# Optimization experiments

Hardware: AMD Instinct MI355X
Metric: run time of the kernel (lower is better)

Reference implementation:

```python
import jax, jax.numpy as jnp
import numpy as np
import math

T, B, V, D = 8, 32, 50257, 256
N = 4096            # memory slots
H = 4               # attention heads
L = 2               # transformer layers
K = 3               # shift width
HALF = K // 2
WIN = 16            # controller window
RH, WH = 1, 1       # read / write heads
EPS = 1e-12


def _pe(win, d):
    pos = jnp.arange(win, dtype=jnp.float32)[:, None]
    div = jnp.exp(jnp.arange(0, d, 2, dtype=jnp.float32) * (-math.log(10000.0) / d))
    pe = jnp.zeros((win, d), dtype=jnp.float32)
    pe = pe.at[:, 0::2].set(jnp.sin(pos * div))
    pe = pe.at[:, 1::2].set(jnp.cos(pos * div))
    return pe[:, None, :]


def _ln(x, g, b, eps=1e-5):
    mu = x.mean(-1, keepdims=True)
    var = ((x - mu) ** 2).mean(-1, keepdims=True)
    return (x - mu) * jax.lax.rsqrt(var + eps) * g + b


def _mha(x, Wqkv, bqkv, Wo, bo):
    S, Bc, Dm = x.shape
    dh = Dm // H
    qkv = x @ Wqkv.T + bqkv
    q, k, v = jnp.split(qkv, 3, axis=-1)
    q = q.reshape(S, Bc, H, dh)
    k = k.reshape(S, Bc, H, dh)
    v = v.reshape(S, Bc, H, dh)
    logits = jnp.einsum('sbhd,tbhd->bhst', q, k) / math.sqrt(dh)
    a = jax.nn.softmax(logits, axis=-1)
    o = jnp.einsum('bhst,tbhd->sbhd', a, v).reshape(S, Bc, Dm)
    return o @ Wo.T + bo


def _addressing(key_v, beta, gate, shift, gamma, prev_w, memory):
    # key_v [B,M], beta/gate/gamma [B,1], shift [B,K], prev_w [B,N], memory [B,N,M]
    key_n = key_v / (jnp.linalg.norm(key_v, axis=-1, keepdims=True) + EPS)
    mem_n = memory / (jnp.linalg.norm(memory, axis=-1, keepdims=True) + EPS)
    cos = jnp.einsum('bnm,bm->bn', mem_n, key_n)
    wc = jax.nn.softmax(jax.nn.softplus(beta) * cos, axis=-1)
    g = jax.nn.sigmoid(gate)
    wg = g * wc + (1.0 - g) * prev_w
    s = jax.nn.softmax(shift, axis=-1)
    shifted = sum(s[:, k:k + 1] * jnp.roll(wg, k - HALF, axis=-1) for k in range(K))
    gp = 1.0 + jax.nn.softplus(gamma)
    wt = (shifted + EPS) ** gp
    return wt / (wt.sum(-1, keepdims=True) + EPS)


def setup_inputs() -> dict:
    key = jax.random.key(0)
    ks = iter(jax.random.split(key, 40))
    def w(shape, s=0.02):
        return jax.random.normal(next(ks), shape, jnp.float32) * s
    return {
        'tokens': jax.random.randint(next(ks), (T, B), 0, V, jnp.int32),
        'emb_W': w((V, D)),
        'read_gate_W': w((D, D)), 'read_gate_b': jnp.zeros((D,)),
        'film_W': w((2 * D, D)), 'film_b': jnp.zeros((2 * D,)),
        't_Wqkv': w((L, 3 * D, D)), 't_bqkv': jnp.zeros((L, 3 * D)),
        't_Wo': w((L, D, D)), 't_bo': jnp.zeros((L, D)),
        't_ln1_g': jnp.ones((L, D)), 't_ln1_b': jnp.zeros((L, D)),
        't_ln2_g': jnp.ones((L, D)), 't_ln2_b': jnp.zeros((L, D)),
        't_W1': w((L, 4 * D, D)), 't_b1': jnp.zeros((L, 4 * D)),
        't_W2': w((L, D, 4 * D)), 't_b2': jnp.zeros((L, D)),
        'out_ln_g': jnp.ones((D,)), 'out_ln_b': jnp.zeros((D,)),
        'lstm_Wih': w((2, 4 * D, D)), 'lstm_Whh': w((2, 4 * D, D)),
        'lstm_bih': jnp.zeros((2, 4 * D)), 'lstm_bhh': jnp.zeros((2, 4 * D)),
        'head_W': w((V, D)), 'head_b': jnp.zeros((V,)),
        'read_W': w((D + 3 + K, D)), 'read_b': jnp.zeros((D + 3 + K,)),
        'write_W': w((3 * D + 3 + K, D)), 'write_b': jnp.zeros((3 * D + 3 + K,)),
    }


def reference(tokens, emb_W, read_gate_W, read_gate_b, film_W, film_b,
              t_Wqkv, t_bqkv, t_Wo, t_bo, t_ln1_g, t_ln1_b, t_ln2_g, t_ln2_b,
              t_W1, t_b1, t_W2, t_b2, out_ln_g, out_ln_b,
              lstm_Wih, lstm_Whh, lstm_bih, lstm_bhh,
              head_W, head_b, read_W, read_b, write_W, write_b):
    pe = _pe(WIN, D)
    memory = jnp.zeros((B, N, D), jnp.float32)
    read_w = jnp.zeros((B, RH, N), jnp.float32).at[:, :, 0].set(1.0)
    write_w = jnp.zeros((B, WH, N), jnp.float32).at[:, :, 0].set(1.0)
    record = jnp.zeros((B, D), jnp.float32)
    hx = jnp.zeros((2, B, D), jnp.float32)
    cx = jnp.zeros((2, B, D), jnp.float32)
    hist = jnp.zeros((1, B, D), jnp.float32)
    logits_all = []
    for t in range(T):  # T fixed, sequential recurrence (context length grows)
        emb = emb_W[tokens[t]]                               # [B,D]
        r = jnp.einsum('bhn,bnm->bm', read_w, memory)        # sum over read heads
        fp = record @ film_W.T + film_b
        gam = 1.0 + jnp.tanh(fp[:, :D])
        bet = fp[:, D:]
        rg = jax.nn.sigmoid(record @ read_gate_W.T + read_gate_b)
        x_in = gam * emb + bet + rg * r
        ctx = jnp.concatenate([hist, x_in[None]], axis=0)
        if ctx.shape[0] > WIN:
            ctx = ctx[-WIN:]
        hist = ctx
        h = ctx + pe[:ctx.shape[0]]
        for l in range(L):  # norm_first pre-LN encoder layers (eval, relu FFN)
            h = h + _mha(_ln(h, t_ln1_g[l], t_ln1_b[l]), t_Wqkv[l], t_bqkv[l], t_Wo[l], t_bo[l])
            h = h + (jax.nn.relu(_ln(h, t_ln2_g[l], t_ln2_b[l]) @ t_W1[l].T + t_b1[l]) @ t_W2[l].T + t_b2[l])
        c_out = _ln(h[-1], out_ln_g, out_ln_b)
        # 2-layer LSTM single step (torch gate order i,f,g,o)
        x_l = c_out
        new_h, new_c = [], []
        for l in range(2):
            gates = x_l @ lstm_Wih[l].T + lstm_bih[l] + hx[l] @ lstm_Whh[l].T + lstm_bhh[l]
            i_g, f_g, g_g, o_g = jnp.split(gates, 4, axis=-1)
            c_new = jax.nn.sigmoid(f_g) * cx[l] + jax.nn.sigmoid(i_g) * jnp.tanh(g_g)
            h_new = jax.nn.sigmoid(o_g) * jnp.tanh(c_new)
            new_h.append(h_new); new_c.append(c_new)
            x_l = h_new
        hx = jnp.stack(new_h); cx = jnp.stack(new_c)
        record = hx[-1]
        c_out = c_out + x_l
        logits_all.append(c_out @ head_W.T + head_b)
        # read addressing
        rp = (c_out @ read_W.T + read_b).reshape(B, RH, -1)
        new_rw = []
        for hh in range(RH):
            p = rp[:, hh]
            new_rw.append(_addressing(p[:, :D], p[:, D:D + 1], p[:, D + 1:D + 2],
                                      p[:, D + 2:D + 2 + K], p[:, D + 2 + K:D + 3 + K],
                                      read_w[:, hh], memory))
        read_w = jnp.stack(new_rw, axis=1)
        # write addressing + erase/add (addressing uses pre-update memory)
        wp = (c_out @ write_W.T + write_b).reshape(B, WH, -1)
        mem_pre = memory
        new_ww = []
        for hh in range(WH):
            p = wp[:, hh]
            wt = _addressing(p[:, :D], p[:, D:D + 1], p[:, D + 1:D + 2],
                             p[:, D + 2:D + 2 + K], p[:, D + 2 + K:D + 3 + K],
                             write_w[:, hh], mem_pre)
            erase = jax.nn.sigmoid(p[:, D + 3 + K:2 * D + 3 + K])
            add = jnp.tanh(p[:, 2 * D + 3 + K:3 * D + 3 + K])
            memory = memory * (1.0 - wt[:, :, None] * erase[:, None, :]) + wt[:, :, None] * add[:, None, :]
            new_ww.append(wt)
        write_w = jnp.stack(new_ww, axis=1)
    return jnp.stack(logits_all, axis=0)  # [T, B, V]
```

## Files before the change

### kernel.cpp

```cpp
#include <hip/hip_runtime.h>
#include <math.h>

#define TT 8
#define BB 32
#define VV 50257
#define DD 256
#define NN 4096
#define EPS_ 1e-12f

typedef __attribute__((ext_vector_type(8))) short short8;
typedef __attribute__((ext_vector_type(4))) float f32x4;

__device__ __forceinline__ float sigf(float x) { return 1.f / (1.f + expf(-x)); }
__device__ __forceinline__ float softplusf_(float x) { return fmaxf(x, 0.f) + log1pf(expf(-fabsf(x))); }
__device__ __forceinline__ unsigned f2bf(float f) {
  union { float f; unsigned u; } c; c.f = f;
  return (c.u + 0x7FFFu + ((c.u >> 16) & 1u)) >> 16;
}
__device__ __forceinline__ float bf2f(unsigned u16) {
  union { unsigned u; float f; } c; c.u = u16 << 16; return c.f;
}

__device__ __forceinline__ float blk_sum(float v, float* s) {
#pragma unroll
// ... 42 lines not shown
  if (k == 0) cb[l * 1024 + np] = bih[l * 1024 + src] + bhh[l * 1024 + src];
}

__global__ void catrw_k(const float* __restrict__ rW, const float* __restrict__ rb,
                        const float* __restrict__ wW, const float* __restrict__ wb,
                        unsigned short* __restrict__ Wrw, float* __restrict__ brw) {
  int i = blockIdx.x * 256 + threadIdx.x;
  if (i >= 1036 * 256) return;
  int k = i & 255, n = i >> 8;
  float v = (n < 262) ? rW[(size_t)n * 256 + k] : wW[(size_t)(n - 262) * 256 + k];
  Wrw[i] = (unsigned short)f2bf(v);
  if (k == 0) brw[n] = (n < 262) ? rb[n] : wb[n - 262];
}

__global__ void brc_k(const float* __restrict__ fb, const float* __restrict__ rb, float* __restrict__ brc) {
  int i = blockIdx.x * 256 + threadIdx.x;
  if (i < 512) brc[i] = fb[i];
  else if (i < 768) brc[i] = rb[i - 512];
}

__global__ __launch_bounds__(256) void ln0_k(const float* __restrict__ hpe,
                                             const float* __restrict__ g1, const float* __restrict__ b1,
                                             unsigned short* __restrict__ q1b) {
  __shared__ float s8[8];
  int b = blockIdx.x, d = threadIdx.x;
  float v = hpe[(size_t)b * 256 + d];
  float mu = blk_sum(v, s8) * (1.f / 256.f);
  float dd = v - mu;
  float var = blk_sum(dd * dd, s8) * (1.f / 256.f);
  float rs = rsqrtf(var + 1e-5f);
  q1b[(size_t)b * 256 + d] = (unsigned short)f2bf(dd * rs * g1[d] + b1[d]);
}

template <int EPI>
__global__ __launch_bounds__(256) void gA_k(const unsigned short* __restrict__ A,
                                            const unsigned short* __restrict__ W,
                                            const float* __restrict__ bias,
                                            float* __restrict__ Cf,
                                            unsigned short* __restrict__ Cb,
                                            int ldc, int Nlim) {
  const int tid = threadIdx.x, w = tid >> 6, l = tid & 63, r = l & 15, q = l >> 4;
  const int m0 = blockIdx.y * 32;
  const int n = blockIdx.x * 64 + w * 16 + r;
  const unsigned short* Ap = A + (size_t)m0 * 256;
  const unsigned short* Wp = W + (size_t)n * 256;
  f32x4 acc0 = {0.f, 0.f, 0.f, 0.f}, acc1 = {0.f, 0.f, 0.f, 0.f};
#pragma unroll
  for (int kt = 0; kt < 8; ++kt) {
    short8 a0 = *(const short8*)(Ap + r * 256 + kt * 32 + q * 8);
    short8 a1 = *(const short8*)(Ap + (16 + r) * 256 + kt * 32 + q * 8);
    short8 bf = *(const short8*)(Wp + kt * 32 + q * 8);
    acc0 = __builtin_amdgcn_mfma_f32_16x16x32_bf16(a0, bf, acc0, 0, 0, 0);
    acc1 = __builtin_amdgcn_mfma_f32_16x16x32_bf16(a1, bf, acc1, 0, 0, 0);
  }
  if (n >= Nlim) return;
  float bb = bias[n];
#pragma unroll
  for (int e = 0; e < 4; ++e) {
    int m1 = m0 + q * 4 + e, m2 = m1 + 16;
    float v1 = acc0[e] + bb, v2 = acc1[e] + bb;
    if constexpr (EPI == 0) {
      Cf[(size_t)m1 * ldc + n] = v1;
      Cf[(size_t)m2 * ldc + n] = v2;
    } else {
      Cb[(size_t)m1 * ldc + n] = (unsigned short)f2bf(fmaxf(v1, 0.f));
      Cb[(size_t)m2 * ldc + n] = (unsigned short)f2bf(fmaxf(v2, 0.f));
    }
  }
}

template <int K, int OLN>
__global__ __launch_bounds__(256) void gB_k(const unsigned short* __restrict__ A,
                                            const unsigned short* __restrict__ W,
                                            const float* __restrict__ bias,
                                            const float* __restrict__ resid,
                                            float* __restrict__ Hout,
                                            const float* __restrict__ lng,
                                            const float* __restrict__ lnb,
                                            unsigned short* __restrict__ Xb, int xstride,
                                            float* __restrict__ c_out) {
  __shared__ float hv[32][260];
  const int tid = threadIdx.x, w = tid >> 6, l = tid & 63, r = l & 15, q = l >> 4;
  const int m0 = blockIdx.x * 32;
  const unsigned short* Ap = A + (size_t)m0 * K;
  const unsigned short* Wp0 = W + (size_t)(w * 64 + 0 + r) * K;
  const unsigned short* Wp1 = W + (size_t)(w * 64 + 16 + r) * K;
  const unsigned short* Wp2 = W + (size_t)(w * 64 + 32 + r) * K;
  const unsigned short* Wp3 = W + (size_t)(w * 64 + 48 + r) * K;
  f32x4 acc0[4], acc1[4];
#pragma unroll
  for (int j = 0; j < 4; ++j) { acc0[j] = {0.f, 0.f, 0.f, 0.f}; acc1[j] = {0.f, 0.f, 0.f, 0.f}; }
#pragma unroll 4
  for (int kt = 0; kt < K / 32; ++kt) {
    short8 a0 = *(const short8*)(Ap + (size_t)r * K + kt * 32 + q * 8);
    short8 a1 = *(const short8*)(Ap + (size_t)(16 + r) * K + kt * 32 + q * 8);
    short8 b0 = *(const short8*)(Wp0 + kt * 32 + q * 8);
    short8 b1 = *(const short8*)(Wp1 + kt * 32 + q * 8);
    short8 b2 = *(const short8*)(Wp2 + kt * 32 + q * 8);
    short8 b3 = *(const short8*)(Wp3 + kt * 32 + q * 8);
    acc0[0] = __builtin_amdgcn_mfma_f32_16x16x32_bf16(a0, b0, acc0[0], 0, 0, 0);
    acc1[0] = __builtin_amdgcn_mfma_f32_16x16x32_bf16(a1, b0, acc1[0], 0, 0, 0);
    acc0[1] = __builtin_amdgcn_mfma_f32_16x16x32_bf16(a0, b1, acc0[1], 0, 0, 0);
    acc1[1] = __builtin_amdgcn_mfma_f32_16x16x32_bf16(a1, b1, acc1[1], 0, 0, 0);
    acc0[2] = __builtin_amdgcn_mfma_f32_16x16x32_bf16(a0, b2, acc0[2], 0, 0, 0);
    acc1[2] = __builtin_amdgcn_mfma_f32_16x16x32_bf16(a1, b2, acc1[2], 0, 0, 0);
    acc0[3] = __builtin_amdgcn_mfma_f32_16x16x32_bf16(a0, b3, acc0[3], 0, 0, 0);
    acc1[3] = __builtin_amdgcn_mfma_f32_16x16x32_bf16(a1, b3, acc1[3], 0, 0, 0);
  }
#pragma unroll
  for (int j = 0; j < 4; ++j) {
    int n = w * 64 + j * 16 + r;
    float bb = bias[n];
#pragma unroll
    for (int e = 0; e < 4; ++e) {
      int m1 = q * 4 + e, m2 = m1 + 16;
      float v1 = acc0[j][e] + bb + resid[(size_t)(m0 + m1) * 256 + n];
      float v2 = acc1[j][e] + bb + resid[(size_t)(m0 + m2) * 256 + n];
      Hout[(size_t)(m0 + m1) * 256 + n] = v1;
      Hout[(size_t)(m0 + m2) * 256 + n] = v2;
      hv[m1][n] = v1;
      hv[m2][n] = v2;
    }
  }
  __syncthreads();
  const float4 g4 = *(const float4*)(lng + l * 4);
  const float4 be4 = *(const float4*)(lnb + l * 4);
#pragma unroll
  for (int i = 0; i < 8; ++i) {
    int row = w * 8 + i;
    float4 v = *(const float4*)&hv[row][l * 4];
    float s1 = v.x + v.y + v.z + v.w;
    float s2 = v.x * v.x + v.y * v.y + v.z * v.z + v.w * v.w;
#pragma unroll
    for (int o = 32; o > 0; o >>= 1) { s1 += __shfl_xor(s1, o); s2 += __shfl_xor(s2, o); }
    float mu = s1 * (1.f / 256.f);
    float var = fmaxf(s2 * (1.f / 256.f) - mu * mu, 0.f);
    float rs = rsqrtf(var + 1e-5f);
    float y0 = (v.x - mu) * rs * g4.x + be4.x;
    float y1 = (v.y - mu) * rs * g4.y + be4.y;
    float y2 = (v.z - mu) * rs * g4.z + be4.z;
    float y3 = (v.w - mu) * rs * g4.w + be4.w;
    uint2 pk;
    pk.x = f2bf(y0) | (f2bf(y1) << 16);
    pk.y = f2bf(y2) | (f2bf(y3) << 16);
    *(uint2*)(Xb + (size_t)(m0 + row) * xstride + l * 4) = pk;
    if constexpr (OLN) {
      float4 cv = make_float4(y0, y1, y2, y3);
      *(float4*)(c_out + (size_t)(m0 + row) * 256 + l * 4) = cv;
    }
  }
}

template <int LAST>
__global__ __launch_bounds__(256) void gL_k(const unsigned short* __restrict__ A,
                                            const unsigned short* __restrict__ W,
                                            const float* __restrict__ cbias,
                                            float* __restrict__ cx,
                                            unsigned short* __restrict__ li_own,
                                            unsigned short* __restrict__ li_next,
                                            const float* __restrict__ c_outp,
                                            unsigned short* __restrict__ cfinb,
                                            unsigned short* __restrict__ record_b) {
  __shared__ float g[32][68];
  const int tid = threadIdx.x, w = tid >> 6, l = tid & 63, r = l & 15, q = l >> 4;
  const int n = blockIdx.x * 64 + w * 16 + r;
  const unsigned short* Wp = W + (size_t)n * 512;
  f32x4 acc0 = {0.f, 0.f, 0.f, 0.f}, acc1 = {0.f, 0.f, 0.f, 0.f};
#pragma unroll 4
  for (int kt = 0; kt < 16; ++kt) {
    short8 a0 = *(const short8*)(A + (size_t)r * 512 + kt * 32 + q * 8);
    short8 a1 = *(const short8*)(A + (size_t)(16 + r) * 512 + kt * 32 + q * 8);
    short8 bf = *(const short8*)(Wp + kt * 32 + q * 8);
    acc0 = __builtin_amdgcn_mfma_f32_16x16x32_bf16(a0, bf, acc0, 0, 0, 0);
    acc1 = __builtin_amdgcn_mfma_f32_16x16x32_bf16(a1, bf, acc1, 0, 0, 0);
  }
  float bb = cbias[n];
  int nb = w * 16 + r;
#pragma unroll
  for (int e = 0; e < 4; ++e) {
    g[q * 4 + e][nb] = acc0[e] + bb;
    g[16 + q * 4 + e][nb] = acc1[e] + bb;
  }
  __syncthreads();
// ... 12 lines not shown
      record_b[b * 256 + dg] = (unsigned short)f2bf(hN);
      cfinb[b * 256 + dg] = (unsigned short)f2bf(c_outp[b * 256 + dg] + hN);
    } else {
      li_next[(size_t)b * 512 + dg] = (unsigned short)f2bf(hN);
    }
  }
}

__global__ __launch_bounds__(256) void xinpw_k(const int* __restrict__ tokens,
                                               const float* __restrict__ embW,
                                               const float* __restrict__ fp,
                                               const float* __restrict__ rvec,
                                               const float* __restrict__ g1, const float* __restrict__ b1,
                                               float* __restrict__ hpe,
                                               unsigned short* __restrict__ q1b, int t) {
  __shared__ float s8[8];
  int b = blockIdx.x, d = threadIdx.x;
  float gam = 1.f + tanhf(fp[(size_t)b * 768 + d]);
  float bet = fp[(size_t)b * 768 + 256 + d];
  float rg = sigf(fp[(size_t)b * 768 + 512 + d]);
  int tok = tokens[t * BB + b];
  float emb = embW[(size_t)tok * 256 + d];
  float ang = (float)(t + 1) * expf(-logf(10000.f) * (float)(d & ~1) / 256.f);
  float pe = (d & 1) ? cosf(ang) : sinf(ang);
  float x = gam * emb + bet + rg * rvec[b * 256 + d] + pe;
  hpe[((size_t)(t + 1) * BB + b) * 256 + d] = x;
  float mu = blk_sum(x, s8) * (1.f / 256.f);
  float dd = x - mu;
  float var = blk_sum(dd * dd, s8) * (1.f / 256.f);
  float rs = rsqrtf(var + 1e-5f);
  q1b[((size_t)(t + 1) * BB + b) * 256 + d] = (unsigned short)f2bf(dd * rs * g1[d] + b1[d]);
}

__global__ __launch_bounds__(128) void attn_k(const float* __restrict__ qkv,
                                              unsigned short* __restrict__ ao, int S) {
  int bh = blockIdx.x;
  int b = bh >> 2, h = bh & 3;
  __shared__ float q[9][64], k[9][64], v[9][64], lg[9][12];
  int tid = threadIdx.x;
  for (int i = tid; i < S * 64; i += 128) {
    int s = i >> 6, d = i & 63;
    const float* base = qkv + (size_t)(s * BB + b) * 768 + h * 64 + d;
    q[s][d] = base[0]; k[s][d] = base[256]; v[s][d] = base[512];
  }
  __syncthreads();
  for (int p = tid; p < S * S; p += 128) {
    int s = p / S, t2 = p % S;
    float acc = 0.f;
    for (int d = 0; d < 64; ++d) acc += q[s][d] * k[t2][d];
    lg[s][t2] = acc * 0.125f;
  }
  __syncthreads();
  if (tid < S) {
    float mx = -1e30f;
    for (int t2 = 0; t2 < S; ++t2) mx = fmaxf(mx, lg[tid][t2]);
    float sum = 0.f;
    for (int t2 = 0; t2 < S; ++t2) { float e = expf(lg[tid][t2] - mx); lg[tid][t2] = e; sum += e; }
    float inv = 1.f / sum;
    for (int t2 = 0; t2 < S; ++t2) lg[tid][t2] *= inv;
  }
  __syncthreads();
  for (int i = tid; i < S * 64; i += 128) {
    int s = i >> 6, d = i & 63;
    float o = 0.f;
    for (int t2 = 0; t2 < S; ++t2) o += lg[s][t2] * v[t2][d];
    ao[(size_t)(s * BB + b) * 256 + h * 64 + d] = (unsigned short)f2bf(o);
  }
}

__global__ __launch_bounds__(64) void attnl_k(const float* __restrict__ qkv,
                                              unsigned short* __restrict__ ao, int S) {
  int bh = blockIdx.x;
  int b = bh >> 2, h = bh & 3;
  int d = threadIdx.x;
  __shared__ float sc[9];
  float qd = qkv[(size_t)((S - 1) * BB + b) * 768 + h * 64 + d];
  for (int j = 0; j < S; ++j) {
    float p = qd * qkv[(size_t)(j * BB + b) * 768 + h * 64 + 256 + d];
#pragma unroll
    for (int o = 32; o > 0; o >>= 1) p += __shfl_down(p, o);
    if (d == 0) sc[j] = p * 0.125f;
  }
  __syncthreads();
  float mx = -1e30f;
  for (int j = 0; j < S; ++j) mx = fmaxf(mx, sc[j]);
  float pj[9], sum = 0.f;
  for (int j = 0; j < S; ++j) { pj[j] = expf(sc[j] - mx); sum += pj[j]; }
  float inv = 1.f / sum;
  float o = 0.f;
  for (int j = 0; j < S; ++j) o += pj[j] * inv * qkv[(size_t)(j * BB + b) * 768 + h * 64 + 512 + d];
  ao[(size_t)b * 256 + h * 64 + d] = (unsigned short)f2bf(o);
}

__global__ __launch_bounds__(256) void head_k(const unsigned short* __restrict__ Wh,
                                              const unsigned short* __restrict__ Ah,
                                              const float* __restrict__ hb,
                                              float* __restrict__ out) {
  const int tid = threadIdx.x;
  const int w = tid >> 6, l = tid & 63;
  const int r = l & 15, q = l >> 4;
  const int n = blockIdx.x * 64 + w * 16 + r;
  const int nc = n < VV ? n : VV - 1;
  const short* Ap = (const short*)Ah;
  const short* Wp = (const short*)Wh + (size_t)nc * 256;
  short8 a0[8], a1[8], bf[8];
#pragma unroll
  for (int kt = 0; kt < 8; ++kt) {
    a0[kt] = *(const short8*)(Ap + r * 256 + kt * 32 + q * 8);
    a1[kt] = *(const short8*)(Ap + (16 + r) * 256 + kt * 32 + q * 8);
    bf[kt] = *(const short8*)(Wp + kt * 32 + q * 8);
  }
  f32x4 acc0 = {0.f, 0.f, 0.f, 0.f}, acc1 = {0.f, 0.f, 0.f, 0.f};
#pragma unroll
  for (int kt = 0; kt < 8; ++kt) {
    acc0 = __builtin_amdgcn_mfma_f32_16x16x32_bf16(a0[kt], bf[kt], acc0, 0, 0, 0);
    acc1 = __builtin_amdgcn_mfma_f32_16x16x32_bf16(a1[kt], bf[kt], acc1, 0, 0, 0);
  }
  if (n < VV) {
    float bb = hb[n];
#pragma unroll
    for (int e = 0; e < 4; ++e) {
      int m = q * 4 + e;
      out[(size_t)m * VV + n] = acc0[e] + bb;
      out[(size_t)(16 + m) * VV + n] = acc1[e] + bb;
    }
  }
}

__global__ __launch_bounds__(256) void passA_k(const unsigned short* __restrict__ mem,
                                               const float* __restrict__ rpwp,
                                               float* __restrict__ dr,
                                               float* __restrict__ dw,
                                               float* __restrict__ nrm) {
  __shared__ float kr[256], kw[256];
  int b = blockIdx.y, tid = threadIdx.x;
  kr[tid] = rpwp[(size_t)b * 1036 + tid];
  kw[tid] = rpwp[(size_t)b * 1036 + 262 + tid];
  __syncthreads();
  int w = tid >> 6, lane = tid & 63;
  float4 kr4 = *(float4*)&kr[lane * 4];
  float4 kw4 = *(float4*)&kw[lane * 4];
  int n0 = blockIdx.x * 16 + w * 4;
  for (int rr = 0; rr < 4; ++rr) {
    int n = n0 + rr;
    const unsigned short* row = mem + ((size_t)b * NN + n) * 256;
    uint2 p = *(const uint2*)(row + lane * 4);
    float m0 = bf2f(p.x & 0xffffu), m1 = bf2f(p.x >> 16);
    float m2 = bf2f(p.y & 0xffffu), m3 = bf2f(p.y >> 16);
    float pr = m0 * kr4.x + m1 * kr4.y + m2 * kr4.z + m3 * kr4.w;
    float pw = m0 * kw4.x + m1 * kw4.y + m2 * kw4.z + m3 * kw4.w;
    float pn = m0 * m0 + m1 * m1 + m2 * m2 + m3 * m3;
#pragma unroll
    for (int o = 32; o > 0; o >>= 1) {
      pr += __shfl_down(pr, o); pw += __shfl_down(pw, o); pn += __shfl_down(pn, o);
    }
    if (lane == 0) {
      dr[(size_t)b * NN + n] = pr;
      dw[(size_t)b * NN + n] = pw;
      nrm[(size_t)b * NN + n] = pn;
    }
  }
}

__global__ __launch_bounds__(256) void addr_k(const float* __restrict__ dr,
                                              const float* __restrict__ dw,
                                              const float* __restrict__ nrm,
                                              const float* __restrict__ rpwp,
                                              float* rw, float* ww,
                                              float* __restrict__ ea,
                                              float* __restrict__ rvec) {
  __shared__ float wg[4096];
  __shared__ float s8[8];
  int head = blockIdx.x & 1, b = blockIdx.x >> 1;
  int tid = threadIdx.x;
  const float* p = rpwp + (size_t)b * 1036 + (head ? 262 : 0);
  const float* dot = (head ? dw : dr) + (size_t)b * NN;
  const float* n2 = nrm + (size_t)b * NN;
  float* wout = (head ? ww : rw) + (size_t)b * NN;

  float kv = p[tid];
  float kn = sqrtf(blk_sum(kv * kv, s8)) + EPS_;
  float beta = p[256], gate = p[257], sh0 = p[258], sh1 = p[259], sh2 = p[260], gamma = p[261];
  float spb = softplusf_(beta);
  float g = sigf(gate);
  float mx3 = fmaxf(sh0, fmaxf(sh1, sh2));
  float e0 = expf(sh0 - mx3), e1 = expf(sh1 - mx3), e2 = expf(sh2 - mx3);
  float esum = e0 + e1 + e2;
  float s0 = e0 / esum, s1 = e1 / esum, s2 = e2 / esum;
  float gp = 1.f + softplusf_(gamma);

  float l[16];
  float lmax = -1e30f;
// ... 115 lines not shown
  const float* head_b = (const float*)d_in[25];
  const float* read_W = (const float*)d_in[26];
  const float* read_b = (const float*)d_in[27];
  const float* write_W = (const float*)d_in[28];
  const float* write_b = (const float*)d_in[29];
  float* out = (float*)d_out;

  float* ws = (float*)d_ws;
  size_t off = 0;
  float* read_w = ws + off; off += (size_t)BB * NN;
  float* write_w = ws + off; off += (size_t)BB * NN;
  float* cx = ws + off; off += 2 * BB * DD;
  float* r_vec = ws + off; off += BB * DD;
  float* dot_r = ws + off; off += (size_t)BB * NN;
  float* dot_w = ws + off; off += (size_t)BB * NN;
  float* norm2 = ws + off; off += (size_t)BB * NN;
  unsigned short* record_b = (unsigned short*)(ws + off); off += BB * DD / 2;
  unsigned short* lstm_in_b = (unsigned short*)(ws + off); off += 2 * BB * 512 / 2;
  size_t zero_floats = off;
  unsigned short* memory = (unsigned short*)(ws + off); off += (size_t)BB * NN * DD / 2;
  float* hpe = ws + off; off += 9 * BB * DD;
  float* h = ws + off; off += 9 * BB * DD;
  float* h2 = ws + off; off += BB * DD;
  float* qkvC = ws + off; off += 9 * BB * 768;
  float* qkv2 = ws + off; off += 9 * BB * 768;
  float* fp = ws + off; off += BB * 768;
  float* c_out = ws + off; off += BB * DD;
  float* rpwp = ws + off; off += BB * 1036;
  float* ea = ws + off; off += BB * 2 * DD;
  unsigned short* q1b = (unsigned short*)(ws + off); off += 9 * BB * DD / 2;
  unsigned short* q2b = (unsigned short*)(ws + off); off += 9 * BB * DD / 2;
  unsigned short* x2b = (unsigned short*)(ws + off); off += 9 * BB * DD / 2;
  unsigned short* x2b2 = (unsigned short*)(ws + off); off += BB * DD / 2;
  unsigned short* ao_b = (unsigned short*)(ws + off); off += 9 * BB * DD / 2;
  unsigned short* ao2_b = (unsigned short*)(ws + off); off += BB * DD / 2;
  unsigned short* mid_b = (unsigned short*)(ws + off); off += 9 * BB * 1024 / 2;
  unsigned short* cfinb = (unsigned short*)(ws + off); off += BB * DD / 2;
  unsigned short* Wh = (unsigned short*)(ws + off); off += (size_t)VV * 256 / 2;
  unsigned short* Wq_b = (unsigned short*)(ws + off); off += 2 * 768 * 256 / 2;
  unsigned short* Wo_b = (unsigned short*)(ws + off); off += 2 * 256 * 256 / 2;
  unsigned short* W1_b = (unsigned short*)(ws + off); off += 2 * 1024 * 256 / 2;
  unsigned short* W2_b = (unsigned short*)(ws + off); off += 2 * 256 * 1024 / 2;
  unsigned short* Wc_b = (unsigned short*)(ws + off); off += 2 * 1024 * 512 / 2;
  unsigned short* Wrw_b = (unsigned short*)(ws + off); off += 1088 * 256 / 2;
  unsigned short* FR_b = (unsigned short*)(ws + off); off += 768 * 256 / 2;
  float* cb2 = ws + off; off += 2 * 1024;
  float* brw = ws + off; off += 1040;
  float* brc = ws + off; off += 768;
  if (ws_size < off * sizeof(float)) return;

  (void)hipMemsetAsync(ws, 0, zero_floats * sizeof(float), stream);
  (void)hipMemsetAsync(Wrw_b + (size_t)1036 * 256, 0, (size_t)52 * 256 * 2, stream);
  init_k<<<32, 256, 0, stream>>>(read_w, write_w, hpe);
  cvtw_k<<<(VV * 256 / 4 + 255) / 256, 256, 0, stream>>>(head_W, Wh, VV * 256 / 4);
  cvtw_k<<<(2 * 768 * 256 / 4 + 255) / 256, 256, 0, stream>>>(t_Wqkv, Wq_b, 2 * 768 * 256 / 4);
  cvtw_k<<<(2 * 256 * 256 / 4 + 255) / 256, 256, 0, stream>>>(t_Wo, Wo_b, 2 * 256 * 256 / 4);
  cvtw_k<<<(2 * 1024 * 256 / 4 + 255) / 256, 256, 0, stream>>>(t_W1, W1_b, 2 * 1024 * 256 / 4);
  cvtw_k<<<(2 * 256 * 1024 / 4 + 255) / 256, 256, 0, stream>>>(t_W2, W2_b, 2 * 256 * 1024 / 4);
  cvtw_k<<<(512 * 256 / 4 + 255) / 256, 256, 0, stream>>>(film_W, FR_b, 512 * 256 / 4);
  cvtw_k<<<(256 * 256 / 4 + 255) / 256, 256, 0, stream>>>(read_gate_W, FR_b + 512 * 256, 256 * 256 / 4);
  catlstm_k<<<4096, 256, 0, stream>>>(lstm_Wih, lstm_Whh, lstm_bih, lstm_bhh, Wc_b, cb2);
  catrw_k<<<1036, 256, 0, stream>>>(read_W, read_b, write_W, write_b, Wrw_b, brw);
  brc_k<<<3, 256, 0, stream>>>(film_b, read_gate_b, brc);
  ln0_k<<<BB, 256, 0, stream>>>(hpe, t_ln1_g, t_ln1_b, q1b);
  gA_k<0><<<dim3(12, 1), 256, 0, stream>>>(q1b, Wq_b, t_bqkv, qkvC, nullptr, 768, 768);

  for (int t = 0; t < TT; ++t) {
    const int S = t + 2;

    gA_k<0><<<dim3(12, 1), 256, 0, stream>>>(record_b, FR_b, brc, fp, nullptr, 768, 768);
    xinpw_k<<<BB, 256, 0, stream>>>(tokens, emb_W, fp, r_vec, t_ln1_g, t_ln1_b, hpe, q1b, t);
    gA_k<0><<<dim3(12, 1), 256, 0, stream>>>(q1b + (size_t)(t + 1) * BB * 256, Wq_b, t_bqkv,
                                             qkvC + (size_t)(t + 1) * BB * 768, nullptr, 768, 768);
    attn_k<<<BB * 4, 128, 0, stream>>>(qkvC, ao_b, S);
    gB_k<256, 0><<<S, 256, 0, stream>>>(ao_b, Wo_b, t_bo, hpe, h, t_ln2_g, t_ln2_b, x2b, 256, nullptr);
    gA_k<1><<<dim3(16, S), 256, 0, stream>>>(x2b, W1_b, t_b1, nullptr, mid_b, 1024, 1024);
    gB_k<1024, 0><<<S, 256, 0, stream>>>(mid_b, W2_b, t_b2, h, h, t_ln1_g + 256, t_ln1_b + 256, q2b, 256, nullptr);

    gA_k<0><<<dim3(12, S), 256, 0, stream>>>(q2b, Wq_b + 768 * 256, t_bqkv + 768, qkv2, nullptr, 768, 768);
    attnl_k<<<BB * 4, 64, 0, stream>>>(qkv2, ao2_b, S);
    gB_k<256, 0><<<1, 256, 0, stream>>>(ao2_b, Wo_b + 256 * 256, t_bo + 256, h + (size_t)(S - 1) * BB * 256,
                                        h2, t_ln2_g + 256, t_ln2_b + 256, x2b2, 256, nullptr);
    gA_k<1><<<dim3(16, 1), 256, 0, stream>>>(x2b2, W1_b + 1024 * 256, t_b1 + 1024, nullptr, mid_b, 1024, 1024);
    gB_k<1024, 1><<<1, 256, 0, stream>>>(mid_b, W2_b + 256 * 1024, t_b2 + 256, h2, h2,
                                         out_ln_g, out_ln_b, lstm_in_b, 512, c_out);

    gL_k<0><<<16, 256, 0, stream>>>(lstm_in_b, Wc_b, cb2, cx, lstm_in_b, lstm_in_b + BB * 512,
                                    nullptr, nullptr, nullptr);
    gL_k<1><<<16, 256, 0, stream>>>(lstm_in_b + BB * 512, Wc_b + (size_t)1024 * 512, cb2 + 1024,
                                    cx + BB * DD, lstm_in_b + BB * 512, nullptr, c_out, cfinb, record_b);

    head_k<<<(VV + 63) / 64, 256, 0, stream>>>(Wh, cfinb, head_b, out + (size_t)t * BB * VV);

    if (t < TT - 1) {
      gA_k<0><<<dim3(17, 1), 256, 0, stream>>>(cfinb, Wrw_b, brw, rpwp, nullptr, 1036, 1036);
      if (t > 0)
        passA_k<<<dim3(NN / 16, BB), 256, 0, stream>>>(memory, rpwp, dot_r, dot_w, norm2);
      addr_k<<<2 * BB, 256, 0, stream>>>(dot_r, dot_w, norm2, rpwp, read_w, write_w, ea, r_vec);
      if (t == 0)
        passB_k<1><<<dim3(NN / 128, BB), 256, 0, stream>>>(memory, write_w, read_w, ea, r_vec);
      else
        passB_k<0><<<dim3(NN / 128, BB), 256, 0, stream>>>(memory, write_w, read_w, ea, r_vec);
    }
  }
}
```

Baseline: 1.679 ms.

## Fuse vocab head with memory pass, split GEMM+LN kernels, merge aux GEMMs

The output-head GEMM and the memory similarity pass (passA) now run as one grid, so the large vocab GEMM overlaps with the memory read. The read/write-param GEMM and the next step's FiLM GEMM are merged into a single launch. The old fused GEMM+LayerNorm kernels, which launched only S blocks, are split into a GEMM spread across 4×S blocks plus a separate LayerNorm kernel. The split adds launches and an extra global round-trip of h, in exchange for more blocks in flight and fewer serial kernels elsewhere.

After: 1.481 ms. -11.8%, faster.

```diff
diff --git a/kernel.cpp b/kernel.cpp
--- a/kernel.cpp
+++ b/kernel.cpp
@@ -98,17 +98,48 @@
   q1b[(size_t)b * 256 + d] = (unsigned short)f2bf(dd * rs * g1[d] + b1[d]);
 }
 
-template <int EPI>
+__device__ __forceinline__ void gA32f_dev(const unsigned short* __restrict__ A,
+                                          const unsigned short* __restrict__ W,
+                                          const float* __restrict__ bias,
+                                          float* __restrict__ Cf, int ldc, int Nlim, int nblk) {
+  const int tid = threadIdx.x, w = tid >> 6, l = tid & 63, r = l & 15, q = l >> 4;
+  const int n = nblk * 64 + w * 16 + r;
+  const unsigned short* Wp = W + (size_t)n * 256;
+  f32x4 acc0 = {0.f, 0.f, 0.f, 0.f}, acc1 = {0.f, 0.f, 0.f, 0.f};
+#pragma unroll
+  for (int kt = 0; kt < 8; ++kt) {
+    short8 a0 = *(const short8*)(A + r * 256 + kt * 32 + q * 8);
+    short8 a1 = *(const short8*)(A + (16 + r) * 256 + kt * 32 + q * 8);
+    short8 bf = *(const short8*)(Wp + kt * 32 + q * 8);
+    acc0 = __builtin_amdgcn_mfma_f32_16x16x32_bf16(a0, bf, acc0, 0, 0, 0);
+    acc1 = __builtin_amdgcn_mfma_f32_16x16x32_bf16(a1, bf, acc1, 0, 0, 0);
+  }
+  if (n >= Nlim) return;
+  float bb = bias[n];
+#pragma unroll
+  for (int e = 0; e < 4; ++e) {
+    int m1 = q * 4 + e, m2 = m1 + 16;
+    Cf[(size_t)m1 * ldc + n] = acc0[e] + bb;
+    Cf[(size_t)m2 * ldc + n] = acc1[e] + bb;
+  }
+}
+
 __global__ __launch_bounds__(256) void gA_k(const unsigned short* __restrict__ A,
                                             const unsigned short* __restrict__ W,
                                             const float* __restrict__ bias,
-                                            float* __restrict__ Cf,
-                                            unsigned short* __restrict__ Cb,
-                                            int ldc, int Nlim) {
+                                            float* __restrict__ Cf, int ldc, int Nlim) {
+  gA32f_dev(A + (size_t)blockIdx.y * 32 * 256, W, bias,
+            Cf + (size_t)blockIdx.y * 32 * ldc, ldc, Nlim, blockIdx.x);
+}
+
+__global__ __launch_bounds__(256) void gAr_k(const unsigned short* __restrict__ A,
+                                             const unsigned short* __restrict__ W,
+                                             const float* __restrict__ bias,
+                                             unsigned short* __restrict__ Cb, int ldc) {
   const int tid = threadIdx.x, w = tid >> 6, l = tid & 63, r = l & 15, q = l >> 4;
-  const int m0 = blockIdx.y * 32;
   const int n = blockIdx.x * 64 + w * 16 + r;
-  const unsigned short* Ap = A + (size_t)m0 * 256;
+  const unsigned short* Ap = A + (size_t)blockIdx.y * 32 * 256;
+  unsigned short* Cp = Cb + (size_t)blockIdx.y * 32 * ldc;
   const unsigned short* Wp = W + (size_t)n * 256;
   f32x4 acc0 = {0.f, 0.f, 0.f, 0.f}, acc1 = {0.f, 0.f, 0.f, 0.f};
 #pragma unroll
@@ -119,82 +150,58 @@
     acc0 = __builtin_amdgcn_mfma_f32_16x16x32_bf16(a0, bf, acc0, 0, 0, 0);
     acc1 = __builtin_amdgcn_mfma_f32_16x16x32_bf16(a1, bf, acc1, 0, 0, 0);
   }
-  if (n >= Nlim) return;
   float bb = bias[n];
 #pragma unroll
   for (int e = 0; e < 4; ++e) {
-    int m1 = m0 + q * 4 + e, m2 = m1 + 16;
-    float v1 = acc0[e] + bb, v2 = acc1[e] + bb;
-    if constexpr (EPI == 0) {
-      Cf[(size_t)m1 * ldc + n] = v1;
-      Cf[(size_t)m2 * ldc + n] = v2;
-    } else {
-      Cb[(size_t)m1 * ldc + n] = (unsigned short)f2bf(fmaxf(v1, 0.f));
-      Cb[(size_t)m2 * ldc + n] = (unsigned short)f2bf(fmaxf(v2, 0.f));
-    }
-  }
-}
-
-template <int K, int OLN>
-__global__ __launch_bounds__(256) void gB_k(const unsigned short* __restrict__ A,
+    int m1 = q * 4 + e, m2 = m1 + 16;
+    Cb[(size_t)(blockIdx.y * 32 + m1) * ldc + n] = (unsigned short)f2bf(fmaxf(acc0[e] + bb, 0.f));
+    Cb[(size_t)(blockIdx.y * 32 + m2) * ldc + n] = (unsigned short)f2bf(fmaxf(acc1[e] + bb, 0.f));
+  }
+  (void)Cp;
+}
+
+template <int K>
+__global__ __launch_bounds__(256) void gC_k(const unsigned short* __restrict__ A,
                                             const unsigned short* __restrict__ W,
                                             const float* __restrict__ bias,
                                             const float* __restrict__ resid,
-                                            float* __restrict__ Hout,
-                                            const float* __restrict__ lng,
-                                            const float* __restrict__ lnb,
-                                            unsigned short* __restrict__ Xb, int xstride,
-                                            float* __restrict__ c_out) {
-  __shared__ float hv[32][260];
+                                            float* __restrict__ Hout) {
   const int tid = threadIdx.x, w = tid >> 6, l = tid & 63, r = l & 15, q = l >> 4;
-  const int m0 = blockIdx.x * 32;
+  const int n = blockIdx.x * 64 + w * 16 + r;
+  const int m0 = blockIdx.y * 32;
   const unsigned short* Ap = A + (size_t)m0 * K;
-  const unsigned short* Wp0 = W + (size_t)(w * 64 + 0 + r) * K;
-  const unsigned short* Wp1 = W + (size_t)(w * 64 + 16 + r) * K;
-  const unsigned short* Wp2 = W + (size_t)(w * 64 + 32 + r) * K;
-  const unsigned short* Wp3 = W + (size_t)(w * 64 + 48 + r) * K;
-  f32x4 acc0[4], acc1[4];
-#pragma unroll
-  for (int j = 0; j < 4; ++j) { acc0[j] = {0.f, 0.f, 0.f, 0.f}; acc1[j] = {0.f, 0.f, 0.f, 0.f}; }
+  const unsigned short* Wp = W + (size_t)n * K;
+  f32x4 acc0 = {0.f, 0.f, 0.f, 0.f}, acc1 = {0.f, 0.f, 0.f, 0.f};
 #pragma unroll 4
   for (int kt = 0; kt < K / 32; ++kt) {
     short8 a0 = *(const short8*)(Ap + (size_t)r * K + kt * 32 + q * 8);
     short8 a1 = *(const short8*)(Ap + (size_t)(16 + r) * K + kt * 32 + q * 8);
-    short8 b0 = *(const short8*)(Wp0 + kt * 32 + q * 8);
-    short8 b1 = *(const short8*)(Wp1 + kt * 32 + q * 8);
-    short8 b2 = *(const short8*)(Wp2 + kt * 32 + q * 8);
-    short8 b3 = *(const short8*)(Wp3 + kt * 32 + q * 8);
-    acc0[0] = __builtin_amdgcn_mfma_f32_16x16x32_bf16(a0, b0, acc0[0], 0, 0, 0);
-    acc1[0] = __builtin_amdgcn_mfma_f32_16x16x32_bf16(a1, b0, acc1[0], 0, 0, 0);
-    acc0[1] = __builtin_amdgcn_mfma_f32_16x16x32_bf16(a0, b1, acc0[1], 0, 0, 0);
-    acc1[1] = __builtin_amdgcn_mfma_f32_16x16x32_bf16(a1, b1, acc1[1], 0, 0, 0);
-    acc0[2] = __builtin_amdgcn_mfma_f32_16x16x32_bf16(a0, b2, acc0[2], 0, 0, 0);
-    acc1[2] = __builtin_amdgcn_mfma_f32_16x16x32_bf16(a1, b2, acc1[2], 0, 0, 0);
-    acc0[3] = __builtin_amdgcn_mfma_f32_16x16x32_bf16(a0, b3, acc0[3], 0, 0, 0);
-    acc1[3] = __builtin_amdgcn_mfma_f32_16x16x32_bf16(a1, b3, acc1[3], 0, 0, 0);
-  }
-#pragma unroll
-  for (int j = 0; j < 4; ++j) {
-    int n = w * 64 + j * 16 + r;
-    float bb = bias[n];
-#pragma unroll
-    for (int e = 0; e < 4; ++e) {
-      int m1 = q * 4 + e, m2 = m1 + 16;
-      float v1 = acc0[j][e] + bb + resid[(size_t)(m0 + m1) * 256 + n];
-      float v2 = acc1[j][e] + bb + resid[(size_t)(m0 + m2) * 256 + n];
-      Hout[(size_t)(m0 + m1) * 256 + n] = v1;
-      Hout[(size_t)(m0 + m2) * 256 + n] = v2;
-      hv[m1][n] = v1;
-      hv[m2][n] = v2;
-    }
-  }
-  __syncthreads();
-  const float4 g4 = *(const float4*)(lng + l * 4);
-  const float4 be4 = *(const float4*)(lnb + l * 4);
+    short8 bf = *(const short8*)(Wp + kt * 32 + q * 8);
+    acc0 = __builtin_amdgcn_mfma_f32_16x16x32_bf16(a0, bf, acc0, 0, 0, 0);
+    acc1 = __builtin_amdgcn_mfma_f32_16x16x32_bf16(a1, bf, acc1, 0, 0, 0);
+  }
+  float bb = bias[n];
+#pragma unroll
+  for (int e = 0; e < 4; ++e) {
+    int m1 = m0 + q * 4 + e, m2 = m1 + 16;
+    Hout[(size_t)m1 * 256 + n] = acc0[e] + bb + resid[(size_t)m1 * 256 + n];
+    Hout[(size_t)m2 * 256 + n] = acc1[e] + bb + resid[(size_t)m2 * 256 + n];
+  }
+}
+
+__global__ __launch_bounds__(256) void addLN_k(const float* __restrict__ H,
+                                               const float* __restrict__ g,
+                                               const float* __restrict__ be,
+                                               unsigned short* __restrict__ Xb, int xstride,
+                                               float* __restrict__ c_out) {
+  const int tid = threadIdx.x, w = tid >> 6, l = tid & 63;
+  const int m0 = blockIdx.x * 32;
+  const float4 g4 = *(const float4*)(g + l * 4);
+  const float4 b4 = *(const float4*)(be + l * 4);
 #pragma unroll
   for (int i = 0; i < 8; ++i) {
-    int row = w * 8 + i;
-    float4 v = *(const float4*)&hv[row][l * 4];
+    int row = m0 + w * 8 + i;
+    float4 v = *(const float4*)(H + (size_t)row * 256 + l * 4);
     float s1 = v.x + v.y + v.z + v.w;
     float s2 = v.x * v.x + v.y * v.y + v.z * v.z + v.w * v.w;
 #pragma unroll
@@ -202,19 +209,89 @@
     float mu = s1 * (1.f / 256.f);
     float var = fmaxf(s2 * (1.f / 256.f) - mu * mu, 0.f);
     float rs = rsqrtf(var + 1e-5f);
-    float y0 = (v.x - mu) * rs * g4.x + be4.x;
-    float y1 = (v.y - mu) * rs * g4.y + be4.y;
-    float y2 = (v.z - mu) * rs * g4.z + be4.z;
-    float y3 = (v.w - mu) * rs * g4.w + be4.w;
+    float y0 = (v.x - mu) * rs * g4.x + b4.x;
+    float y1 = (v.y - mu) * rs * g4.y + b4.y;
+    float y2 = (v.z - mu) * rs * g4.z + b4.z;
+    float y3 = (v.w - mu) * rs * g4.w + b4.w;
     uint2 pk;
     pk.x = f2bf(y0) | (f2bf(y1) << 16);
     pk.y = f2bf(y2) | (f2bf(y3) << 16);
-    *(uint2*)(Xb + (size_t)(m0 + row) * xstride + l * 4) = pk;
-    if constexpr (OLN) {
+    *(uint2*)(Xb + (size_t)row * xstride + l * 4) = pk;
+    if (c_out) {
       float4 cv = make_float4(y0, y1, y2, y3);
-      *(float4*)(c_out + (size_t)(m0 + row) * 256 + l * 4) = cv;
-    }
-  }
+      *(float4*)(c_out + (size_t)row * 256 + l * 4) = cv;
+    }
+  }
+}
+
+__global__ __launch_bounds__(256) void auxg_k(const unsigned short* __restrict__ cfinb,
+                                              const unsigned short* __restrict__ Wrw,
+                                              const float* __restrict__ brw, float* __restrict__ rpwp,
+                                              const unsigned short* __restrict__ record_b,
+                                              const unsigned short* __restrict__ FRw,
+                                              const float* __restrict__ brc, float* __restrict__ fp) {
+  if (blockIdx.x < 17) gA32f_dev(cfinb, Wrw, brw, rpwp, 1036, 1036, blockIdx.x);
+  else gA32f_dev(record_b, FRw, brc, fp, 768, 768, blockIdx.x - 17);
+}
+
+__global__ __launch_bounds__(128) void attn_k(const float* __restrict__ qkv,
+                                              unsigned short* __restrict__ ao, int S) {
+  int bh = blockIdx.x;
+  int b = bh >> 2, h = bh & 3;
+  __shared__ float q[9][64], k[9][64], v[9][64], lg[9][12];
+  int tid = threadIdx.x;
+  for (int i = tid; i < S * 64; i += 128) {
+    int s = i >> 6, d = i & 63;
+    const float* base = qkv + (size_t)(s * BB + b) * 768 + h * 64 + d;
+    q[s][d] = base[0]; k[s][d] = base[256]; v[s][d] = base[512];
+  }
+  __syncthreads();
+  for (int p = tid; p < S * S; p += 128) {
+    int s = p / S, t2 = p % S;
+    float acc = 0.f;
+    for (int d = 0; d < 64; ++d) acc += q[s][d] * k[t2][d];
+    lg[s][t2] = acc * 0.125f;
+  }
+  __syncthreads();
+  if (tid < S) {
+    float mx = -1e30f;
+    for (int t2 = 0; t2 < S; ++t2) mx = fmaxf(mx, lg[tid][t2]);
+    float sum = 0.f;
+    for (int t2 = 0; t2 < S; ++t2) { float e = expf(lg[tid][t2] - mx); lg[tid][t2] = e; sum += e; }
+    float inv = 1.f / sum;
+    for (int t2 = 0; t2 < S; ++t2) lg[tid][t2] *= inv;
+  }
+  __syncthreads();
+  for (int i = tid; i < S * 64; i += 128) {
+    int s = i >> 6, d = i & 63;
+    float o = 0.f;
+    for (int t2 = 0; t2 < S; ++t2) o += lg[s][t2] * v[t2][d];
+    ao[(size_t)(s * BB + b) * 256 + h * 64 + d] = (unsigned short)f2bf(o);
+  }
+}
+
+__global__ __launch_bounds__(64) void attnl_k(const float* __restrict__ qkv,
+                                              unsigned short* __restrict__ ao, int S) {
+  int bh = blockIdx.x;
+  int b = bh >> 2, h = bh & 3;
+  int d = threadIdx.x;
+  __shared__ float sc[9];
+  float qd = qkv[(size_t)((S - 1) * BB + b) * 768 + h * 64 + d];
+  for (int j = 0; j < S; ++j) {
+    float p = qd * qkv[(size_t)(j * BB + b) * 768 + h * 64 + 256 + d];
+#pragma unroll
+    for (int o = 32; o > 0; o >>= 1) p += __shfl_down(p, o);
+    if (d == 0) sc[j] = p * 0.125f;
+  }
+  __syncthreads();
+  float mx = -1e30f;
+  for (int j = 0; j < S; ++j) mx = fmaxf(mx, sc[j]);
+  float pj[9], sum = 0.f;
+  for (int j = 0; j < S; ++j) { pj[j] = expf(sc[j] - mx); sum += pj[j]; }
+  float inv = 1.f / sum;
+  float o = 0.f;
+  for (int j = 0; j < S; ++j) o += pj[j] * inv * qkv[(size_t)(j * BB + b) * 768 + h * 64 + 512 + d];
+  ao[(size_t)b * 256 + h * 64 + d] = (unsigned short)f2bf(o);
 }
 
 template <int LAST>
@@ -293,121 +370,64 @@
   q1b[((size_t)(t + 1) * BB + b) * 256 + d] = (unsigned short)f2bf(dd * rs * g1[d] + b1[d]);
 }
 
-__global__ __launch_bounds__(128) void attn_k(const float* __restrict__ qkv,
-                                              unsigned short* __restrict__ ao, int S) {
-  int bh = blockIdx.x;
-  int b = bh >> 2, h = bh & 3;
-  __shared__ float q[9][64], k[9][64], v[9][64], lg[9][12];
-  int tid = threadIdx.x;
-  for (int i = tid; i < S * 64; i += 128) {
-    int s = i >> 6, d = i & 63;
-    const float* base = qkv + (size_t)(s * BB + b) * 768 + h * 64 + d;
-    q[s][d] = base[0]; k[s][d] = base[256]; v[s][d] = base[512];
-  }
-  __syncthreads();
-  for (int p = tid; p < S * S; p += 128) {
-    int s = p / S, t2 = p % S;
-    float acc = 0.f;
-    for (int d = 0; d < 64; ++d) acc += q[s][d] * k[t2][d];
-    lg[s][t2] = acc * 0.125f;
-  }
-  __syncthreads();
-  if (tid < S) {
-    float mx = -1e30f;
-    for (int t2 = 0; t2 < S; ++t2) mx = fmaxf(mx, lg[tid][t2]);
-    float sum = 0.f;
-    for (int t2 = 0; t2 < S; ++t2) { float e = expf(lg[tid][t2] - mx); lg[tid][t2] = e; sum += e; }
-    float inv = 1.f / sum;
-    for (int t2 = 0; t2 < S; ++t2) lg[tid][t2] *= inv;
-  }
-  __syncthreads();
-  for (int i = tid; i < S * 64; i += 128) {
-    int s = i >> 6, d = i & 63;
-    float o = 0.f;
-    for (int t2 = 0; t2 < S; ++t2) o += lg[s][t2] * v[t2][d];
-    ao[(size_t)(s * BB + b) * 256 + h * 64 + d] = (unsigned short)f2bf(o);
-  }
-}
-
-__global__ __launch_bounds__(64) void attnl_k(const float* __restrict__ qkv,
-                                              unsigned short* __restrict__ ao, int S) {
-  int bh = blockIdx.x;
-  int b = bh >> 2, h = bh & 3;
-  int d = threadIdx.x;
-  __shared__ float sc[9];
-  float qd = qkv[(size_t)((S - 1) * BB + b) * 768 + h * 64 + d];
-  for (int j = 0; j < S; ++j) {
-    float p = qd * qkv[(size_t)(j * BB + b) * 768 + h * 64 + 256 + d];
-#pragma unroll
-    for (int o = 32; o > 0; o >>= 1) p += __shfl_down(p, o);
-    if (d == 0) sc[j] = p * 0.125f;
-  }
-  __syncthreads();
-  float mx = -1e30f;
-  for (int j = 0; j < S; ++j) mx = fmaxf(mx, sc[j]);
-  float pj[9], sum = 0.f;
-  for (int j = 0; j < S; ++j) { pj[j] = expf(sc[j] - mx); sum += pj[j]; }
-  float inv = 1.f / sum;
-  float o = 0.f;
-  for (int j = 0; j < S; ++j) o += pj[j] * inv * qkv[(size_t)(j * BB + b) * 768 + h * 64 + 512 + d];
-  ao[(size_t)b * 256 + h * 64 + d] = (unsigned short)f2bf(o);
-}
-
-__global__ __launch_bounds__(256) void head_k(const unsigned short* __restrict__ Wh,
-                                              const unsigned short* __restrict__ Ah,
-                                              const float* __restrict__ hb,
-                                              float* __restrict__ out) {
+__global__ __launch_bounds__(256) void fusePA_k(const unsigned short* __restrict__ Wh,
+                                                const unsigned short* __restrict__ Ah,
+                                                const float* __restrict__ hb,
+                                                float* __restrict__ out,
+                                                const unsigned short* __restrict__ mem,
+                                                const float* __restrict__ rpwp,
+                                                float* __restrict__ dr,
+                                                float* __restrict__ dw,
+                                                float* __restrict__ nrm) {
+  __shared__ float kr[256], kw[256];
+  const int bid = blockIdx.x;
   const int tid = threadIdx.x;
-  const int w = tid >> 6, l = tid & 63;
-  const int r = l & 15, q = l >> 4;
-  const int n = blockIdx.x * 64 + w * 16 + r;
-  const int nc = n < VV ? n : VV - 1;
-  const short* Ap = (const short*)Ah;
-  const short* Wp = (const short*)Wh + (size_t)nc * 256;
-  short8 a0[8], a1[8], bf[8];
-#pragma unroll
-  for (int kt = 0; kt < 8; ++kt) {
-    a0[kt] = *(const short8*)(Ap + r * 256 + kt * 32 + q * 8);
-    a1[kt] = *(const short8*)(Ap + (16 + r) * 256 + kt * 32 + q * 8);
-    bf[kt] = *(const short8*)(Wp + kt * 32 + q * 8);
-  }
-  f32x4 acc0 = {0.f, 0.f, 0.f, 0.f}, acc1 = {0.f, 0.f, 0.f, 0.f};
-#pragma unroll
-  for (int kt = 0; kt < 8; ++kt) {
-    acc0 = __builtin_amdgcn_mfma_f32_16x16x32_bf16(a0[kt], bf[kt], acc0, 0, 0, 0);
-    acc1 = __builtin_amdgcn_mfma_f32_16x16x32_bf16(a1[kt], bf[kt], acc1, 0, 0, 0);
-  }
-  if (n < VV) {
-    float bb = hb[n];
-#pragma unroll
-    for (int e = 0; e < 4; ++e) {
-      int m = q * 4 + e;
-      out[(size_t)m * VV + n] = acc0[e] + bb;
-      out[(size_t)(16 + m) * VV + n] = acc1[e] + bb;
-    }
-  }
-}
-
-__global__ __launch_bounds__(256) void passA_k(const unsigned short* __restrict__ mem,
-                                               const float* __restrict__ rpwp,
-                                               float* __restrict__ dr,
-                                               float* __restrict__ dw,
-                                               float* __restrict__ nrm) {
-  __shared__ float kr[256], kw[256];
-  int b = blockIdx.y, tid = threadIdx.x;
-  kr[tid] = rpwp[(size_t)b * 1036 + tid];
-  kw[tid] = rpwp[(size_t)b * 1036 + 262 + tid];
+  if (bid < 786) {
+    const int w = tid >> 6, l = tid & 63;
+    const int r = l & 15, q = l >> 4;
+    const int n = bid * 64 + w * 16 + r;
+    const int nc = n < VV ? n : VV - 1;
+    const short* Ap = (const short*)Ah;
+    const short* Wp = (const short*)Wh + (size_t)nc * 256;
+    short8 a0[8], a1[8], bf[8];
+#pragma unroll
+    for (int kt = 0; kt < 8; ++kt) {
+      a0[kt] = *(const short8*)(Ap + r * 256 + kt * 32 + q * 8);
+      a1[kt] = *(const short8*)(Ap + (16 + r) * 256 + kt * 32 + q * 8);
+      bf[kt] = *(const short8*)(Wp + kt * 32 + q * 8);
+    }
+    f32x4 acc0 = {0.f, 0.f, 0.f, 0.f}, acc1 = {0.f, 0.f, 0.f, 0.f};
+#pragma unroll
+    for (int kt = 0; kt < 8; ++kt) {
+      acc0 = __builtin_amdgcn_mfma_f32_16x16x32_bf16(a0[kt], bf[kt], acc0, 0, 0, 0);
+      acc1 = __builtin_amdgcn_mfma_f32_16x16x32_bf16(a1[kt], bf[kt], acc1, 0, 0, 0);
+    }
+    if (n < VV) {
+      float bb = hb[n];
+#pragma unroll
+      for (int e = 0; e < 4; ++e) {
+        int m = q * 4 + e;
+        out[(size_t)m * VV + n] = acc0[e] + bb;
+        out[(size_t)(16 + m) * VV + n] = acc1[e] + bb;
+      }
+    }
+    return;
+  }
+  const int idx = bid - 786;
+  const int bx = idx & 255, by = idx >> 8;
+  kr[tid] = rpwp[(size_t)by * 1036 + tid];
+  kw[tid] = rpwp[(size_t)by * 1036 + 262 + tid];
   __syncthreads();
   int w = tid >> 6, lane = tid & 63;
   float4 kr4 = *(float4*)&kr[lane * 4];
   float4 kw4 = *(float4*)&kw[lane * 4];
-  int n0 = blockIdx.x * 16 + w * 4;
+  int n0 = bx * 16 + w * 4;
   for (int rr = 0; rr < 4; ++rr) {
     int n = n0 + rr;
-    const unsigned short* row = mem + ((size_t)b * NN + n) * 256;
-    uint2 p = *(const uint2*)(row + lane * 4);
-    float m0 = bf2f(p.x & 0xffffu), m1 = bf2f(p.x >> 16);
-    float m2 = bf2f(p.y & 0xffffu), m3 = bf2f(p.y >> 16);
+    const unsigned short* row = mem + ((size_t)by * NN + n) * 256;
+    uint2 pck = *(const uint2*)(row + lane * 4);
+    float m0 = bf2f(pck.x & 0xffffu), m1 = bf2f(pck.x >> 16);
+    float m2 = bf2f(pck.y & 0xffffu), m3 = bf2f(pck.y >> 16);
     float pr = m0 * kr4.x + m1 * kr4.y + m2 * kr4.z + m3 * kr4.w;
     float pw = m0 * kw4.x + m1 * kw4.y + m2 * kw4.z + m3 * kw4.w;
     float pn = m0 * m0 + m1 * m1 + m2 * m2 + m3 * m3;
@@ -416,9 +436,9 @@
       pr += __shfl_down(pr, o); pw += __shfl_down(pw, o); pn += __shfl_down(pn, o);
     }
     if (lane == 0) {
-      dr[(size_t)b * NN + n] = pr;
-      dw[(size_t)b * NN + n] = pw;
-      nrm[(size_t)b * NN + n] = pn;
+      dr[(size_t)by * NN + n] = pr;
+      dw[(size_t)by * NN + n] = pw;
+      nrm[(size_t)by * NN + n] = pn;
     }
   }
 }
@@ -600,7 +620,7 @@
   unsigned short* q2b = (unsigned short*)(ws + off); off += 9 * BB * DD / 2;
   unsigned short* x2b = (unsigned short*)(ws + off); off += 9 * BB * DD / 2;
   unsigned short* x2b2 = (unsigned short*)(ws + off); off += BB * DD / 2;
-  unsigned short* ao_b = (unsigned short*)(ws + off); off += 9 * BB * DD / 2;
+  unsigned short* ao1_b = (unsigned short*)(ws + off); off += 9 * BB * DD / 2;
   unsigned short* ao2_b = (unsigned short*)(ws + off); off += BB * DD / 2;
   unsigned short* mid_b = (unsigned short*)(ws + off); off += 9 * BB * 1024 / 2;
   unsigned short* cfinb = (unsigned short*)(ws + off); off += BB * DD / 2;
@@ -631,44 +651,49 @@
   catrw_k<<<1036, 256, 0, stream>>>(read_W, read_b, write_W, write_b, Wrw_b, brw);
   brc_k<<<3, 256, 0, stream>>>(film_b, read_gate_b, brc);
   ln0_k<<<BB, 256, 0, stream>>>(hpe, t_ln1_g, t_ln1_b, q1b);
-  gA_k<0><<<dim3(12, 1), 256, 0, stream>>>(q1b, Wq_b, t_bqkv, qkvC, nullptr, 768, 768);
+  gA_k<<<dim3(12, 1), 256, 0, stream>>>(q1b, Wq_b, t_bqkv, qkvC, 768, 768);
+  gA_k<<<dim3(12, 1), 256, 0, stream>>>(record_b, FR_b, brc, fp, 768, 768);
 
   for (int t = 0; t < TT; ++t) {
     const int S = t + 2;
 
-    gA_k<0><<<dim3(12, 1), 256, 0, stream>>>(record_b, FR_b, brc, fp, nullptr, 768, 768);
     xinpw_k<<<BB, 256, 0, stream>>>(tokens, emb_W, fp, r_vec, t_ln1_g, t_ln1_b, hpe, q1b, t);
-    gA_k<0><<<dim3(12, 1), 256, 0, stream>>>(q1b + (size_t)(t + 1) * BB * 256, Wq_b, t_bqkv,
-                                             qkvC + (size_t)(t + 1) * BB * 768, nullptr, 768, 768);
-    attn_k<<<BB * 4, 128, 0, stream>>>(qkvC, ao_b, S);
-    gB_k<256, 0><<<S, 256, 0, stream>>>(ao_b, Wo_b, t_bo, hpe, h, t_ln2_g, t_ln2_b, x2b, 256, nullptr);
-    gA_k<1><<<dim3(16, S), 256, 0, stream>>>(x2b, W1_b, t_b1, nullptr, mid_b, 1024, 1024);
-    gB_k<1024, 0><<<S, 256, 0, stream>>>(mid_b, W2_b, t_b2, h, h, t_ln1_g + 256, t_ln1_b + 256, q2b, 256, nullptr);
-
-    gA_k<0><<<dim3(12, S), 256, 0, stream>>>(q2b, Wq_b + 768 * 256, t_bqkv + 768, qkv2, nullptr, 768, 768);
+    gA_k<<<dim3(12, 1), 256, 0, stream>>>(q1b + (size_t)(t + 1) * BB * 256, Wq_b, t_bqkv,
+                                          qkvC + (size_t)(t + 1) * BB * 768, 768, 768);
+    attn_k<<<BB * 4, 128, 0, stream>>>(qkvC, ao1_b, S);
+    gC_k<256><<<dim3(4, S), 256, 0, stream>>>(ao1_b, Wo_b, t_bo, hpe, h);
+    addLN_k<<<S, 256, 0, stream>>>(h, t_ln2_g, t_ln2_b, x2b, 256, nullptr);
+    gAr_k<<<dim3(16, S), 256, 0, stream>>>(x2b, W1_b, t_b1, mid_b, 1024);
+    gC_k<1024><<<dim3(4, S), 256, 0, stream>>>(mid_b, W2_b, t_b2, h, h);
+    addLN_k<<<S, 256, 0, stream>>>(h, t_ln1_g + 256, t_ln1_b + 256, q2b, 256, nullptr);
+    gA_k<<<dim3(12, S), 256, 0, stream>>>(q2b, Wq_b + 768 * 256, t_bqkv + 768, qkv2, 768, 768);
     attnl_k<<<BB * 4, 64, 0, stream>>>(qkv2, ao2_b, S);
-    gB_k<256, 0><<<1, 256, 0, stream>>>(ao2_b, Wo_b + 256 * 256, t_bo + 256, h + (size_t)(S - 1) * BB * 256,
-                                        h2, t_ln2_g + 256, t_ln2_b + 256, x2b2, 256, nullptr);
-    gA_k<1><<<dim3(16, 1), 256, 0, stream>>>(x2b2, W1_b + 1024 * 256, t_b1 + 1024, nullptr, mid_b, 1024, 1024);
-    gB_k<1024, 1><<<1, 256, 0, stream>>>(mid_b, W2_b + 256 * 1024, t_b2 + 256, h2, h2,
-                                         out_ln_g, out_ln_b, lstm_in_b, 512, c_out);
-
+    gC_k<256><<<dim3(4, 1), 256, 0, stream>>>(ao2_b, Wo_b + 256 * 256, t_bo + 256,
+                                              h + (size_t)(S - 1) * BB * 256, h2);
+    addLN_k<<<1, 256, 0, stream>>>(h2, t_ln2_g + 256, t_ln2_b + 256, x2b2, 256, nullptr);
+    gAr_k<<<dim3(16, 1), 256, 0, stream>>>(x2b2, W1_b + 1024 * 256, t_b1 + 1024, mid_b, 1024);
+    gC_k<1024><<<dim3(4, 1), 256, 0, stream>>>(mid_b, W2_b + 256 * 1024, t_b2 + 256, h2, h2);
+    addLN_k<<<1, 256, 0, stream>>>(h2, out_ln_g, out_ln_b, lstm_in_b, 512, c_out);
     gL_k<0><<<16, 256, 0, stream>>>(lstm_in_b, Wc_b, cb2, cx, lstm_in_b, lstm_in_b + BB * 512,
                                     nullptr, nullptr, nullptr);
     gL_k<1><<<16, 256, 0, stream>>>(lstm_in_b + BB * 512, Wc_b + (size_t)1024 * 512, cb2 + 1024,
                                     cx + BB * DD, lstm_in_b + BB * 512, nullptr, c_out, cfinb, record_b);
-
-    head_k<<<(VV + 63) / 64, 256, 0, stream>>>(Wh, cfinb, head_b, out + (size_t)t * BB * VV);
-
     if (t < TT - 1) {
-      gA_k<0><<<dim3(17, 1), 256, 0, stream>>>(cfinb, Wrw_b, brw, rpwp, nullptr, 1036, 1036);
+      auxg_k<<<29, 256, 0, stream>>>(cfinb, Wrw_b, brw, rpwp, record_b, FR_b, brc, fp);
       if (t > 0)
-        passA_k<<<dim3(NN / 16, BB), 256, 0, stream>>>(memory, rpwp, dot_r, dot_w, norm2);
+        fusePA_k<<<786 + 8192, 256, 0, stream>>>(Wh, cfinb, head_b, out + (size_t)t * BB * VV,
+                                                 memory, rpwp, dot_r, dot_w, norm2);
+      else
+        fusePA_k<<<786, 256, 0, stream>>>(Wh, cfinb, head_b, out + (size_t)t * BB * VV,
+                                          memory, rpwp, dot_r, dot_w, norm2);
       addr_k<<<2 * BB, 256, 0, stream>>>(dot_r, dot_w, norm2, rpwp, read_w, write_w, ea, r_vec);
       if (t == 0)
         passB_k<1><<<dim3(NN / 128, BB), 256, 0, stream>>>(memory, write_w, read_w, ea, r_vec);
       else
         passB_k<0><<<dim3(NN / 128, BB), 256, 0, stream>>>(memory, write_w, read_w, ea, r_vec);
-    }
-  }
-}
+    } else {
+      fusePA_k<<<786, 256, 0, stream>>>(Wh, cfinb, head_b, out + (size_t)t * BB * VV,
+                                        memory, rpwp, dot_r, dot_w, norm2);
+    }
+  }
+}
```
